# Optimization experiments

Hardware: AMD Instinct MI355X
Metric: run time of the kernel (lower is better)

Reference implementation:

```python
import jax, jax.numpy as jnp
import numpy as np

N = 100000   # nodes
E = 1600000  # edges
G = 64       # graphs in batch
F_IN = 128
H = 128
SV = 64
AD = 32


def setup_inputs() -> dict:
    key = jax.random.key(0)
    ks = jax.random.split(key, 12)
    s = 0.05
    return {
        "x": jax.random.normal(ks[0], (N, F_IN), jnp.float32),
        "edge_index": jax.random.randint(ks[1], (2, E), 0, N, dtype=jnp.int64),
        "batch": jnp.sort(jax.random.randint(ks[2], (N,), 0, G, dtype=jnp.int64)),
        "state_vector": jax.random.normal(ks[3], (G, SV), jnp.float32),
        "action": jax.random.normal(ks[4], (G, AD), jnp.float32),
        "W1": jax.random.normal(ks[5], (F_IN, H), jnp.float32) * s,
        "b1": jnp.zeros((H,), jnp.float32),
        "W2": jax.random.normal(ks[6], (H, H), jnp.float32) * s,
        "b2": jnp.zeros((H,), jnp.float32),
        "Wf1": jax.random.normal(ks[7], (H + SV + AD, 256), jnp.float32) * s,
        "bf1": jnp.zeros((256,), jnp.float32),
        "Wf2": jax.random.normal(ks[8], (256, 256), jnp.float32) * s,
        "bf2": jnp.zeros((256,), jnp.float32),
        "Wo": jax.random.normal(ks[9], (256, 1), jnp.float32) * s,
        "bo": jnp.zeros((1,), jnp.float32),
    }


def gcn_conv(x, W, b, src, dst, deg_inv_sqrt):
    # PyG GCNConv: h = x @ W; aggregate D^-1/2 (A+I) D^-1/2 h; + b
    h = x @ W
    norm = deg_inv_sqrt[src] * deg_inv_sqrt[dst]          # [E]
    agg = jax.ops.segment_sum(h[src] * norm[:, None], dst, num_segments=N)
    agg = agg + h * (deg_inv_sqrt * deg_inv_sqrt)[:, None]  # self loops
    return agg + b


def reference(x, edge_index, batch, state_vector, action,
              W1, b1, W2, b2, Wf1, bf1, Wf2, bf2, Wo, bo):
    src, dst = edge_index[0], edge_index[1]
    # degree after adding self loops (aggregation index = dst, PyG default flow)
    deg = jax.ops.segment_sum(jnp.ones((E,), jnp.float32), dst, num_segments=N) + 1.0
    deg_inv_sqrt = jax.lax.rsqrt(deg)

    h = jax.nn.relu(gcn_conv(x, W1, b1, src, dst, deg_inv_sqrt))
    h = jax.nn.relu(gcn_conv(h, W2, b2, src, dst, deg_inv_sqrt))

    # global_mean_pool over graph ids
    sums = jax.ops.segment_sum(h, batch, num_segments=G)
    cnts = jax.ops.segment_sum(jnp.ones((N,), jnp.float32), batch, num_segments=G)
    pooled = sums / jnp.maximum(cnts, 1.0)[:, None]       # [G, H]

    z = jnp.concatenate([pooled, state_vector, action], axis=1)  # [G, H+SV+AD]
    z = jax.nn.relu(z @ Wf1 + bf1)
    z = jax.nn.relu(z @ Wf2 + bf2)
    return z @ Wo + bo                                     # [G, 1]
```

## Files before the change

kernel.cpp:

```cpp
#include <hip/hip_runtime.h>
#include <hip/hip_bf16.h>
#include <stdint.h>

#define N_NODES 100000
#define N_EDGES 1600000
#define N_GRAPHS 64
#define HDIM 128

#define BUCKET_SHIFT 9
#define NBUCK ((N_NODES + 511) >> 9)
#define CAP 9216
#define SCAT_CHUNK 4096
#define SCAT_NBLK ((N_EDGES + SCAT_CHUNK - 1) / SCAT_CHUNK)

typedef __bf16 bf16x8 __attribute__((ext_vector_type(8)));
typedef float f32x4 __attribute__((ext_vector_type(4)));
typedef float f32x2 __attribute__((ext_vector_type(2)));

__global__ void init_kernel(int* __restrict__ gcur, float* __restrict__ psum) {
    int i = blockIdx.x * blockDim.x + threadIdx.x;
    if (i < NBUCK) gcur[i] = i * CAP;
    int j = i - NBUCK;
    if (j >= 0 && j < N_GRAPHS * HDIM) psum[j] = 0.f;
}

__global__ __launch_bounds__(256) void transpose_w2_kernel(const float* __restrict__ W1,
                                                           const float* __restrict__ W2,
                                                           __hip_bfloat16* __restrict__ Wt1,
                                                           __hip_bfloat16* __restrict__ Wt2) {
    int bid = blockIdx.x;
    const float* W = (bid < 64) ? W1 : W2;
    __hip_bfloat16* Wt = (bid < 64) ? Wt1 : Wt2;
    int bb = bid & 63;
    int n = bb * 2 + (threadIdx.x >> 7);
    int k = threadIdx.x & 127;
    Wt[n * 128 + k] = __float2bfloat16(W[k * 128 + n]);
}

__global__ __launch_bounds__(256) void scatter_kernel(const int* __restrict__ src,
                                                      const int* __restrict__ dst,
                                                      int* __restrict__ gcur,
                                                      int* __restrict__ sorted, int E) {
    __shared__ int hist[NBUCK];
    __shared__ int base_s[NBUCK];
    int tid = threadIdx.x;
    int e0 = blockIdx.x * SCAT_CHUNK;
    int sv[SCAT_CHUNK / 256], dv[SCAT_CHUNK / 256];
#pragma unroll
    for (int j = 0; j < SCAT_CHUNK / 256; j++) {
        int e = e0 + (j << 8) + tid;
        if (e < E) { sv[j] = src[e]; dv[j] = dst[e]; } else { sv[j] = -1; dv[j] = -1; }
    }
    if (tid < NBUCK) hist[tid] = 0;
    __syncthreads();
#pragma unroll
    for (int j = 0; j < SCAT_CHUNK / 256; j++)
        if (dv[j] >= 0) atomicAdd(&hist[dv[j] >> BUCKET_SHIFT], 1);
    __syncthreads();
    if (tid < NBUCK) {
        int c = hist[tid];
        base_s[tid] = (c > 0) ? atomicAdd(&gcur[tid], c) : 0;
    }
    __syncthreads();
    if (tid < NBUCK) hist[tid] = 0;
    __syncthreads();
#pragma unroll
    for (int j = 0; j < SCAT_CHUNK / 256; j++) {
        if (dv[j] >= 0) {
            int b = dv[j] >> BUCKET_SHIFT;
            int idx = atomicAdd(&hist[b], 1);
            sorted[base_s[b] + idx] = ((dv[j] & 511) << 17) | sv[j];
        }
    }
}

__global__ __launch_bounds__(256) void bucket_build_kernel(const int* __restrict__ sorted,
                                                           const int* __restrict__ gcur,
                                                           int2* __restrict__ rs2,
                                                           float* __restrict__ dis,
                                                           int* __restrict__ csr_src) {
    __shared__ int cnt[512];
    __shared__ int excl[512];
    __shared__ int ps[256];
    int b = blockIdx.x, tid = threadIdx.x;
    cnt[tid] = 0; cnt[tid + 256] = 0;
    __syncthreads();
    int node0 = b << BUCKET_SHIFT;
    int lo = b * CAP, hi = gcur[b];
    for (int i = lo + tid; i < hi; i += 256)
        atomicAdd(&cnt[((unsigned)sorted[i]) >> 17], 1);
    __syncthreads();
    int c0 = cnt[2 * tid], c1 = cnt[2 * tid + 1];
    ps[tid] = c0 + c1;
    __syncthreads();
#pragma unroll
    for (int off = 1; off < 256; off <<= 1) {
        int t = (tid >= off) ? ps[tid - off] : 0;
        __syncthreads();
        ps[tid] += t;
        __syncthreads();
    }
    int pex = ps[tid] - (c0 + c1);
    excl[2 * tid] = pex;
    excl[2 * tid + 1] = pex + c0;
    __syncthreads();
#pragma unroll
    for (int k = 0; k < 2; k++) {
        int li = tid + k * 256;
        int node = node0 + li;
        if (node < N_NODES) {
            int st = lo + excl[li];
            int c = cnt[li];
            rs2[node] = make_int2(st, st + c);
            dis[node] = rsqrtf((float)c + 1.0f);
        }
    }
    cnt[tid] = 0; cnt[tid + 256] = 0;
    __syncthreads();
    for (int i = lo + tid; i < hi; i += 256) {
        int v = sorted[i];
        int li = ((unsigned)v) >> 17;
        int idx = atomicAdd(&cnt[li], 1);
        csr_src[lo + excl[li] + idx] = v & 0x1FFFF;
    }
}

__global__ void graph_bounds_kernel(const int* __restrict__ batch, int* __restrict__ gstart,
                                    int n, int G) {
    int i = blockIdx.x * blockDim.x + threadIdx.x;
    if (i >= n) return;
    int b = batch[i];
    int prev = (i == 0) ? -1 : batch[i - 1];
    for (int g = prev + 1; g <= b; ++g) gstart[g] = i;
    if (i == n - 1) {
        for (int g = b + 1; g <= G; ++g) gstart[g] = n;
    }
}

template<bool A_FP32>
__global__ __launch_bounds__(256) void gemm_mfma_kernel(const void* __restrict__ Av,
                                                        const __hip_bfloat16* __restrict__ Wt,
                                                        const float* __restrict__ scale,
                                                        unsigned char* __restrict__ C, int nrows) {
    __shared__ float Cs[64 * 132];
    int tid = threadIdx.x;
    int wave = tid >> 6, lane = tid & 63;
    int quad = lane >> 4, l16 = lane & 15;
    int row0 = blockIdx.x * 64;
    int arow = row0 + wave * 16 + l16;
    int arow_c = min(arow, nrows - 1);

    const __hip_bfloat16* A16 = (const __hip_bfloat16*)Av;
    const float* A32 = (const float*)Av;

    f32x4 acc[8];
#pragma unroll
    for (int t = 0; t < 8; t++) acc[t] = (f32x4){0.f, 0.f, 0.f, 0.f};

#pragma unroll
    for (int kt = 0; kt < 4; kt++) {
        int kbase = kt * 32 + quad * 8;
        union { bf16x8 v; __hip_bfloat16 h[8]; uint4 u; } au;
        if (A_FP32) {
            const float* ap = A32 + (size_t)arow_c * 128 + kbase;
            float4 u0 = *(const float4*)ap;
            float4 u1 = *(const float4*)(ap + 4);
            au.h[0] = __float2bfloat16(u0.x); au.h[1] = __float2bfloat16(u0.y);
            au.h[2] = __float2bfloat16(u0.z); au.h[3] = __float2bfloat16(u0.w);
            au.h[4] = __float2bfloat16(u1.x); au.h[5] = __float2bfloat16(u1.y);
            au.h[6] = __float2bfloat16(u1.z); au.h[7] = __float2bfloat16(u1.w);
        } else {
            au.u = *(const uint4*)(A16 + (size_t)arow_c * 128 + kbase);
        }
#pragma unroll
        for (int t = 0; t < 8; t++) {
            bf16x8 b = *(const bf16x8*)(Wt + (size_t)(t * 16 + l16) * 128 + kbase);
            acc[t] = __builtin_amdgcn_mfma_f32_16x16x32_bf16(au.v, b, acc[t], 0, 0, 0);
        }
    }

    int rbase = wave * 16 + quad * 4;
    float s[4];
#pragma unroll
    for (int r = 0; r < 4; r++) s[r] = scale[min(row0 + rbase + r, nrows - 1)];
#pragma unroll
    for (int t = 0; t < 8; t++) {
#pragma unroll
        for (int r = 0; r < 4; r++)
            Cs[(rbase + r) * 132 + t * 16 + l16] = acc[t][r] * s[r];
    }
    __syncthreads();

#pragma unroll
    for (int p = 0; p < 4; p++) {
        int g = p * 256 + tid;
        int row = g >> 4, c8 = (g & 15) * 8;
        int grow = row0 + row;
        if (grow < nrows) {
            const float* cp = &Cs[row * 132 + c8];
            float4 v0 = *(const float4*)cp;
            float4 v1 = *(const float4*)(cp + 4);
            int w0 = __builtin_amdgcn_cvt_pk_fp8_f32(v0.x, v0.y, 0, false);
            w0 = __builtin_amdgcn_cvt_pk_fp8_f32(v0.z, v0.w, w0, true);
            int w1 = __builtin_amdgcn_cvt_pk_fp8_f32(v1.x, v1.y, 0, false);
            w1 = __builtin_amdgcn_cvt_pk_fp8_f32(v1.z, v1.w, w1, true);
            *(uint2*)(C + (size_t)grow * 128 + c8) = make_uint2((unsigned)w0, (unsigned)w1);
        }
    }
}

__global__ __launch_bounds__(256) void agg_kernel(const unsigned char* __restrict__ h8,
                                                  const float* __restrict__ dis,
                                                  const int2* __restrict__ rs2,
                                                  const int* __restrict__ csr_src,
                                                  const float* __restrict__ bias,
                                                  __hip_bfloat16* __restrict__ out, int n) {
    int node = blockIdx.x * 4 + (threadIdx.x >> 6);
    if (node >= n) return;
    int lane = threadIdx.x & 63;
    int q = lane >> 4, f = lane & 15;
    float acc[8];
#pragma unroll
    for (int j = 0; j < 8; j++) acc[j] = 0.f;
    int2 se = rs2[node];
    int i = se.x, i1 = se.y;
    for (; i + 4 <= i1; i += 4) {
        int s = csr_src[i + q];
        uint2 u = *(const uint2*)(h8 + (size_t)s * 128 + f * 8);
        f32x2 d0 = __builtin_amdgcn_cvt_pk_f32_fp8((int)u.x, false);
        f32x2 d1 = __builtin_amdgcn_cvt_pk_f32_fp8((int)u.x, true);
        f32x2 d2 = __builtin_amdgcn_cvt_pk_f32_fp8((int)u.y, false);
        f32x2 d3 = __builtin_amdgcn_cvt_pk_f32_fp8((int)u.y, true);
        acc[0] += d0[0]; acc[1] += d0[1]; acc[2] += d1[0]; acc[3] += d1[1];
        acc[4] += d2[0]; acc[5] += d2[1]; acc[6] += d3[0]; acc[7] += d3[1];
    }
    if (i < i1) {
        bool valid = (i + q) < i1;
        int e = valid ? (i + q) : (i1 - 1);
        int s = csr_src[e];
        uint2 u = *(const uint2*)(h8 + (size_t)s * 128 + f * 8);
        if (valid) {
            f32x2 d0 = __builtin_amdgcn_cvt_pk_f32_fp8((int)u.x, false);
            f32x2 d1 = __builtin_amdgcn_cvt_pk_f32_fp8((int)u.x, true);
            f32x2 d2 = __builtin_amdgcn_cvt_pk_f32_fp8((int)u.y, false);
            f32x2 d3 = __builtin_amdgcn_cvt_pk_f32_fp8((int)u.y, true);
            acc[0] += d0[0]; acc[1] += d0[1]; acc[2] += d1[0]; acc[3] += d1[1];
            acc[4] += d2[0]; acc[5] += d2[1]; acc[6] += d3[0]; acc[7] += d3[1];
        }
    }
    if (q == 0) {
        uint2 u = *(const uint2*)(h8 + (size_t)node * 128 + f * 8);
        f32x2 d0 = __builtin_amdgcn_cvt_pk_f32_fp8((int)u.x, false);
        f32x2 d1 = __builtin_amdgcn_cvt_pk_f32_fp8((int)u.x, true);
        f32x2 d2 = __builtin_amdgcn_cvt_pk_f32_fp8((int)u.y, false);
        f32x2 d3 = __builtin_amdgcn_cvt_pk_f32_fp8((int)u.y, true);
        acc[0] += d0[0]; acc[1] += d0[1]; acc[2] += d1[0]; acc[3] += d1[1];
        acc[4] += d2[0]; acc[5] += d2[1]; acc[6] += d3[0]; acc[7] += d3[1];
    }
#pragma unroll
    for (int j = 0; j < 8; j++) {
        float v = acc[j];
        v += __shfl_down(v, 32, 64);
        v += __shfl_down(v, 16, 64);
        acc[j] = v;
    }
    if (q == 0) {
        float dn = dis[node];
        float4 b0 = *(const float4*)(bias + f * 8);
        float4 b1 = *(const float4*)(bias + f * 8 + 4);
        float r0 = fmaxf(fmaf(acc[0], dn, b0.x), 0.f);
        float r1 = fmaxf(fmaf(acc[1], dn, b0.y), 0.f);
        float r2 = fmaxf(fmaf(acc[2], dn, b0.z), 0.f);
        float r3 = fmaxf(fmaf(acc[3], dn, b0.w), 0.f);
        float r4 = fmaxf(fmaf(acc[4], dn, b1.x), 0.f);
        float r5 = fmaxf(fmaf(acc[5], dn, b1.y), 0.f);
        float r6 = fmaxf(fmaf(acc[6], dn, b1.z), 0.f);
        float r7 = fmaxf(fmaf(acc[7], dn, b1.w), 0.f);
        __hip_bfloat162 p0 = __float22bfloat162_rn(make_float2(r0, r1));
        __hip_bfloat162 p1 = __float22bfloat162_rn(make_float2(r2, r3));
        __hip_bfloat162 p2 = __float22bfloat162_rn(make_float2(r4, r5));
        __hip_bfloat162 p3 = __float22bfloat162_rn(make_float2(r6, r7));
        uint4 pk;
        pk.x = *(unsigned int*)&p0; pk.y = *(unsigned int*)&p1;
        pk.z = *(unsigned int*)&p2; pk.w = *(unsigned int*)&p3;
        *(uint4*)(out + (size_t)node * 128 + f * 8) = pk;
    }
}

#define POOL_ROWS 128
__global__ __launch_bounds__(256) void pool_kernel(const __hip_bfloat16* __restrict__ h,
                                                   const int* __restrict__ batch,
                                                   const int* __restrict__ gstart,
                                                   float* __restrict__ psum, int n) {
    __shared__ float red[16 * 128];
    int tid = threadIdx.x;
    int rr = tid >> 4, fg = tid & 15;
    int r0 = blockIdx.x * POOL_ROWS;
    if (r0 >= n) return;
    int r1 = min(n, r0 + POOL_ROWS);
    int g = batch[r0];
    int seg_lo = r0;
    while (seg_lo < r1) {
        while (gstart[g + 1] <= seg_lo) g++;
        int seg_hi = min(r1, gstart[g + 1]);
        float a[8];
#pragma unroll
        for (int j = 0; j < 8; j++) a[j] = 0.f;
        for (int r = seg_lo + rr; r < seg_hi; r += 16) {
            uint4 u = *(const uint4*)(h + (size_t)r * 128 + fg * 8);
            float2 f0 = __bfloat1622float2(*(__hip_bfloat162*)&u.x);
            float2 f1 = __bfloat1622float2(*(__hip_bfloat162*)&u.y);
            float2 f2 = __bfloat1622float2(*(__hip_bfloat162*)&u.z);
            float2 f3 = __bfloat1622float2(*(__hip_bfloat162*)&u.w);
            a[0] += f0.x; a[1] += f0.y; a[2] += f1.x; a[3] += f1.y;
            a[4] += f2.x; a[5] += f2.y; a[6] += f3.x; a[7] += f3.y;
        }
        *(float4*)&red[rr * 128 + fg * 8] = make_float4(a[0], a[1], a[2], a[3]);
        *(float4*)&red[rr * 128 + fg * 8 + 4] = make_float4(a[4], a[5], a[6], a[7]);
        __syncthreads();
        if (tid < 128) {
            float s = 0.f;
#pragma unroll
            for (int k = 0; k < 16; k++) s += red[k * 128 + tid];
            atomicAdd(&psum[g * 128 + tid], s);
        }
        __syncthreads();
        seg_lo = seg_hi;
    }
}

__global__ __launch_bounds__(256) void mlp_kernel(const float* __restrict__ psum,
                                                  const int* __restrict__ gstart,
                                                  const float* __restrict__ sv,
                                                  const float* __restrict__ act,
                                                  const float* __restrict__ Wf1,
                                                  const float* __restrict__ bf1,
                                                  const float* __restrict__ Wf2,
                                                  const float* __restrict__ bf2,
                                                  const float* __restrict__ Wo,
                                                  const float* __restrict__ bo,
                                                  float* __restrict__ out) {
    int g = blockIdx.x, tid = threadIdx.x;
    __shared__ float z[224];
    __shared__ float z1[256];
    __shared__ float red[256];
    if (tid < 128) {
        int c = gstart[g + 1] - gstart[g];
        float cnt = fmaxf((float)c, 1.f);
        z[tid] = psum[g * 128 + tid] / cnt;
    } else if (tid < 192) {
        z[tid] = sv[g * 64 + (tid - 128)];
    } else if (tid < 224) {
        z[tid] = act[g * 32 + (tid - 192)];
    }
    __syncthreads();
    float a = bf1[tid];
    for (int k = 0; k < 224; k++) a = fmaf(z[k], Wf1[k * 256 + tid], a);
    z1[tid] = fmaxf(a, 0.f);
    __syncthreads();
    float b = bf2[tid];
    for (int k = 0; k < 256; k++) b = fmaf(z1[k], Wf2[k * 256 + tid], b);
    b = fmaxf(b, 0.f);
    red[tid] = b * Wo[tid];
    __syncthreads();
    for (int off = 128; off > 0; off >>= 1) {
        if (tid < off) red[tid] += red[tid + off];
        __syncthreads();
    }
    if (tid == 0) out[g] = red[0] + bo[0];
}

extern "C" void kernel_launch(void* const* d_in, const int* in_sizes, int n_in,
                              void* d_out, int out_size, void* d_ws, size_t ws_size,
                              hipStream_t stream) {
    const float* x   = (const float*)d_in[0];
    const int*   eidx = (const int*)d_in[1];
    const int*   batch = (const int*)d_in[2];
    const float* sv  = (const float*)d_in[3];
    const float* act = (const float*)d_in[4];
    const float* W1  = (const float*)d_in[5];
    const float* b1  = (const float*)d_in[6];
    const float* W2  = (const float*)d_in[7];
    const float* b2  = (const float*)d_in[8];
    const float* Wf1 = (const float*)d_in[9];
    const float* bf1 = (const float*)d_in[10];
    const float* Wf2 = (const float*)d_in[11];
    const float* bf2 = (const float*)d_in[12];
    const float* Wo  = (const float*)d_in[13];
    const float* bo  = (const float*)d_in[14];
    float* out = (float*)d_out;

    const int* srcp = eidx;
    const int* dstp = eidx + N_EDGES;

    char* w = (char*)d_ws;
    int* gcur = (int*)w;               w += (size_t)NBUCK * 4;
    float* psum = (float*)w;           w += (size_t)N_GRAPHS * HDIM * 4;
    int2* rs2 = (int2*)w;              w += (size_t)N_NODES * 8;
    float* dis = (float*)w;            w += (size_t)N_NODES * 4;
    int* gstart = (int*)w;             w += (size_t)(N_GRAPHS + 1) * 4;
    w = (char*)(((uintptr_t)w + 255) & ~(uintptr_t)255);
    int* csr_src = (int*)w;            w += (size_t)NBUCK * CAP * 4;
    w = (char*)(((uintptr_t)w + 255) & ~(uintptr_t)255);
    int* sorted = (int*)w;             w += (size_t)NBUCK * CAP * 4;
    w = (char*)(((uintptr_t)w + 255) & ~(uintptr_t)255);
    __hip_bfloat16* Wt1 = (__hip_bfloat16*)w;   w += (size_t)HDIM * HDIM * 2;
    __hip_bfloat16* Wt2 = (__hip_bfloat16*)w;   w += (size_t)HDIM * HDIM * 2;
    w = (char*)(((uintptr_t)w + 255) & ~(uintptr_t)255);
    unsigned char* hbuf = (unsigned char*)w;    w += (size_t)N_NODES * HDIM;
    w = (char*)(((uintptr_t)w + 255) & ~(uintptr_t)255);
    __hip_bfloat16* abuf = (__hip_bfloat16*)w;  w += (size_t)N_NODES * HDIM * 2;

    init_kernel<<<(NBUCK + N_GRAPHS * HDIM + 255) / 256, 256, 0, stream>>>(gcur, psum);
    transpose_w2_kernel<<<128, 256, 0, stream>>>(W1, W2, Wt1, Wt2);

    scatter_kernel<<<SCAT_NBLK, 256, 0, stream>>>(srcp, dstp, gcur, sorted, N_EDGES);
    bucket_build_kernel<<<NBUCK, 256, 0, stream>>>(sorted, gcur, rs2, dis, csr_src);
    graph_bounds_kernel<<<(N_NODES + 255) / 256, 256, 0, stream>>>(batch, gstart, N_NODES, N_GRAPHS);

    int gemm_blocks = (N_NODES + 63) / 64;
    int agg_blocks = (N_NODES + 3) / 4;

    gemm_mfma_kernel<true><<<gemm_blocks, 256, 0, stream>>>(x, Wt1, dis, hbuf, N_NODES);
    agg_kernel<<<agg_blocks, 256, 0, stream>>>(hbuf, dis, rs2, csr_src, b1, abuf, N_NODES);
    gemm_mfma_kernel<false><<<gemm_blocks, 256, 0, stream>>>(abuf, Wt2, dis, hbuf, N_NODES);
    agg_kernel<<<agg_blocks, 256, 0, stream>>>(hbuf, dis, rs2, csr_src, b2, abuf, N_NODES);

    pool_kernel<<<(N_NODES + POOL_ROWS - 1) / POOL_ROWS, 256, 0, stream>>>(abuf, batch, gstart, psum, N_NODES);
    mlp_kernel<<<N_GRAPHS, 256, 0, stream>>>(psum, gstart, sv, act, Wf1, bf1, Wf2, bf2, Wo, bo, out);
}
```

Baseline: 363.6 us.

## Split each node's edge aggregation across two waves with two loads in flight

The aggregation kernel now assigns two wavefronts per node instead of one. Each wave handles alternating groups of four edges and issues two independent gathers per loop iteration. The partial sums are combined through shared memory after a block barrier. The aim is more memory-level parallelism for the latency-bound gathers, at the cost of twice the waves, a __syncthreads, and an LDS round trip per node.

```diff
diff --git a/kernel.cpp b/kernel.cpp
--- a/kernel.cpp
+++ b/kernel.cpp
@@ -209,53 +209,60 @@
     }
 }
 
+__device__ __forceinline__ void accum8(float* acc, uint2 u) {
+    f32x2 d0 = __builtin_amdgcn_cvt_pk_f32_fp8((int)u.x, false);
+    f32x2 d1 = __builtin_amdgcn_cvt_pk_f32_fp8((int)u.x, true);
+    f32x2 d2 = __builtin_amdgcn_cvt_pk_f32_fp8((int)u.y, false);
+    f32x2 d3 = __builtin_amdgcn_cvt_pk_f32_fp8((int)u.y, true);
+    acc[0] += d0[0]; acc[1] += d0[1]; acc[2] += d1[0]; acc[3] += d1[1];
+    acc[4] += d2[0]; acc[5] += d2[1]; acc[6] += d3[0]; acc[7] += d3[1];
+}
+
 __global__ __launch_bounds__(256) void agg_kernel(const unsigned char* __restrict__ h8,
                                                   const float* __restrict__ dis,
                                                   const int2* __restrict__ rs2,
                                                   const int* __restrict__ csr_src,
                                                   const float* __restrict__ bias,
                                                   __hip_bfloat16* __restrict__ out, int n) {
-    int node = blockIdx.x * 4 + (threadIdx.x >> 6);
-    if (node >= n) return;
-    int lane = threadIdx.x & 63;
+    __shared__ float part[2][128];
+    int tid = threadIdx.x;
+    int wave = tid >> 6;
+    int nib = wave >> 1;
+    int w = wave & 1;
+    int node = blockIdx.x * 2 + nib;
+    int lane = tid & 63;
     int q = lane >> 4, f = lane & 15;
     float acc[8];
 #pragma unroll
     for (int j = 0; j < 8; j++) acc[j] = 0.f;
-    int2 se = rs2[node];
-    int i = se.x, i1 = se.y;
-    for (; i + 4 <= i1; i += 4) {
-        int s = csr_src[i + q];
+
+    bool nvalid = node < n;
+    int i0 = 0, i1 = 0;
+    if (nvalid) { int2 se = rs2[node]; i0 = se.x; i1 = se.y; }
+    int ng = (i1 - i0 + 3) >> 2;
+
+    int g = w;
+    for (; g + 2 < ng; g += 4) {
+        int e1 = i0 + (g << 2) + q;
+        int e2 = i0 + ((g + 2) << 2) + q;
+        bool v2 = e2 < i1;
+        int s1 = csr_src[e1];
+        int s2 = csr_src[v2 ? e2 : i0];
+        uint2 u1 = *(const uint2*)(h8 + (size_t)s1 * 128 + f * 8);
+        uint2 u2 = *(const uint2*)(h8 + (size_t)s2 * 128 + f * 8);
+        accum8(acc, u1);
+        if (v2) accum8(acc, u2);
+    }
+    for (; g < ng; g += 2) {
+        int e = i0 + (g << 2) + q;
+        bool v = e < i1;
+        int s = csr_src[v ? e : i0];
         uint2 u = *(const uint2*)(h8 + (size_t)s * 128 + f * 8);
-        f32x2 d0 = __builtin_amdgcn_cvt_pk_f32_fp8((int)u.x, false);
-        f32x2 d1 = __builtin_amdgcn_cvt_pk_f32_fp8((int)u.x, true);
-        f32x2 d2 = __builtin_amdgcn_cvt_pk_f32_fp8((int)u.y, false);
-        f32x2 d3 = __builtin_amdgcn_cvt_pk_f32_fp8((int)u.y, true);
-        acc[0] += d0[0]; acc[1] += d0[1]; acc[2] += d1[0]; acc[3] += d1[1];
-        acc[4] += d2[0]; acc[5] += d2[1]; acc[6] += d3[0]; acc[7] += d3[1];
-    }
-    if (i < i1) {
-        bool valid = (i + q) < i1;
-        int e = valid ? (i + q) : (i1 - 1);
-        int s = csr_src[e];
-        uint2 u = *(const uint2*)(h8 + (size_t)s * 128 + f * 8);
-        if (valid) {
-            f32x2 d0 = __builtin_amdgcn_cvt_pk_f32_fp8((int)u.x, false);
-            f32x2 d1 = __builtin_amdgcn_cvt_pk_f32_fp8((int)u.x, true);
-            f32x2 d2 = __builtin_amdgcn_cvt_pk_f32_fp8((int)u.y, false);
-            f32x2 d3 = __builtin_amdgcn_cvt_pk_f32_fp8((int)u.y, true);
-            acc[0] += d0[0]; acc[1] += d0[1]; acc[2] += d1[0]; acc[3] += d1[1];
-            acc[4] += d2[0]; acc[5] += d2[1]; acc[6] += d3[0]; acc[7] += d3[1];
-        }
-    }
-    if (q == 0) {
+        if (v) accum8(acc, u);
+    }
+    if (w == 0 && nvalid) {
         uint2 u = *(const uint2*)(h8 + (size_t)node * 128 + f * 8);
-        f32x2 d0 = __builtin_amdgcn_cvt_pk_f32_fp8((int)u.x, false);
-        f32x2 d1 = __builtin_amdgcn_cvt_pk_f32_fp8((int)u.x, true);
-        f32x2 d2 = __builtin_amdgcn_cvt_pk_f32_fp8((int)u.y, false);
-        f32x2 d3 = __builtin_amdgcn_cvt_pk_f32_fp8((int)u.y, true);
-        acc[0] += d0[0]; acc[1] += d0[1]; acc[2] += d1[0]; acc[3] += d1[1];
-        acc[4] += d2[0]; acc[5] += d2[1]; acc[6] += d3[0]; acc[7] += d3[1];
+        if (q == 0) accum8(acc, u);
     }
 #pragma unroll
     for (int j = 0; j < 8; j++) {
@@ -264,18 +271,25 @@
         v += __shfl_down(v, 16, 64);
         acc[j] = v;
     }
-    if (q == 0) {
+    if (w == 1 && q == 0) {
+        *(float4*)&part[nib][f * 8] = make_float4(acc[0], acc[1], acc[2], acc[3]);
+        *(float4*)&part[nib][f * 8 + 4] = make_float4(acc[4], acc[5], acc[6], acc[7]);
+    }
+    __syncthreads();
+    if (w == 0 && q == 0 && nvalid) {
+        float4 pa = *(const float4*)&part[nib][f * 8];
+        float4 pb = *(const float4*)&part[nib][f * 8 + 4];
         float dn = dis[node];
         float4 b0 = *(const float4*)(bias + f * 8);
         float4 b1 = *(const float4*)(bias + f * 8 + 4);
-        float r0 = fmaxf(fmaf(acc[0], dn, b0.x), 0.f);
-        float r1 = fmaxf(fmaf(acc[1], dn, b0.y), 0.f);
-        float r2 = fmaxf(fmaf(acc[2], dn, b0.z), 0.f);
-        float r3 = fmaxf(fmaf(acc[3], dn, b0.w), 0.f);
-        float r4 = fmaxf(fmaf(acc[4], dn, b1.x), 0.f);
-        float r5 = fmaxf(fmaf(acc[5], dn, b1.y), 0.f);
-        float r6 = fmaxf(fmaf(acc[6], dn, b1.z), 0.f);
-        float r7 = fmaxf(fmaf(acc[7], dn, b1.w), 0.f);
+        float r0 = fmaxf(fmaf(acc[0] + pa.x, dn, b0.x), 0.f);
+        float r1 = fmaxf(fmaf(acc[1] + pa.y, dn, b0.y), 0.f);
+        float r2 = fmaxf(fmaf(acc[2] + pa.z, dn, b0.z), 0.f);
+        float r3 = fmaxf(fmaf(acc[3] + pa.w, dn, b0.w), 0.f);
+        float r4 = fmaxf(fmaf(acc[4] + pb.x, dn, b1.x), 0.f);
+        float r5 = fmaxf(fmaf(acc[5] + pb.y, dn, b1.y), 0.f);
+        float r6 = fmaxf(fmaf(acc[6] + pb.z, dn, b1.z), 0.f);
+        float r7 = fmaxf(fmaf(acc[7] + pb.w, dn, b1.w), 0.f);
         __hip_bfloat162 p0 = __float22bfloat162_rn(make_float2(r0, r1));
         __hip_bfloat162 p1 = __float22bfloat162_rn(make_float2(r2, r3));
         __hip_bfloat162 p2 = __float22bfloat162_rn(make_float2(r4, r5));
@@ -419,7 +433,7 @@
     graph_bounds_kernel<<<(N_NODES + 255) / 256, 256, 0, stream>>>(batch, gstart, N_NODES, N_GRAPHS);
 
     int gemm_blocks = (N_NODES + 63) / 64;
-    int agg_blocks = (N_NODES + 3) / 4;
+    int agg_blocks = (N_NODES + 1) / 2;
 
     gemm_mfma_kernel<true><<<gemm_blocks, 256, 0, stream>>>(x, Wt1, dis, hbuf, N_NODES);
     agg_kernel<<<agg_blocks, 256, 0, stream>>>(hbuf, dis, rs2, csr_src, b1, abuf, N_NODES);
```

Measured after the change: 408.8 us. 1.12x slower.
